# Kernel tuning notes

Measured on AMD Instinct MI355X. Metric: run time of the kernel, lower is better.

## Reference

```python
import jax, jax.numpy as jnp
import numpy as np

B, L, E, H, D, DFF = 2, 2048, 1024, 16, 64, 4096
SCALE = D ** 0.5


def rmsnorm(x):
    # NOTE: original uses mean(x*x)**0.5 with no eps and no learned scale
    rms = jnp.sqrt(jnp.mean(x * x, axis=-1, keepdims=True))
    return x / rms


def alibi_matrix():
    i = jnp.arange(L)
    dists = -jnp.abs(i[None, :] - i[:, None]).astype(jnp.float32)  # [L, L]
    slopes = 2.0 ** (-jnp.linspace(1.0, 8.0, H))                   # [H]
    alibi = slopes[:, None, None] * dists                          # [H, L, L]
    causal = jnp.tril(jnp.ones((L, L), dtype=bool))
    return jnp.where(causal[None], alibi, -jnp.inf)[None]          # [1, H, L, L]


def setup_inputs() -> dict:
    key = jax.random.key(0)
    ks = jax.random.split(key, 16)
    s = 0.02
    return {
        "X": jax.random.normal(ks[0], (B, L, E), jnp.float32),
        "encoder_out": jax.random.normal(ks[1], (B, L, E), jnp.float32),
        # self-attention params
        "Wqkv": jax.random.normal(ks[2], (E, 3 * H * D), jnp.float32) * s,
        "bqkv": jnp.zeros((3 * H * D,), jnp.float32),
        "Wo_sa": jax.random.normal(ks[3], (H * D, E), jnp.float32) * s,
        "bo_sa": jnp.zeros((E,), jnp.float32),
        # cross-attention params (computed by torch module but its forward returns X, so unused)
        "Wq": jax.random.normal(ks[4], (E, H * D), jnp.float32) * s,
        "bq": jnp.zeros((H * D,), jnp.float32),
        "Wkv": jax.random.normal(ks[5], (E, 2 * H * D), jnp.float32) * s,
        "bkv": jnp.zeros((2 * H * D,), jnp.float32),
        "Wo_ca": jax.random.normal(ks[6], (H * D, E), jnp.float32) * s,
        "bo_ca": jnp.zeros((E,), jnp.float32),
        # GLU FFN params (bias=False)
        "Ww": jax.random.normal(ks[7], (E, DFF), jnp.float32) * s,
        "Wv": jax.random.normal(ks[8], (E, DFF), jnp.float32) * s,
        "Wout": jax.random.normal(ks[9], (DFF, E), jnp.float32) * s,
    }


def reference(X, encoder_out, Wqkv, bqkv, Wo_sa, bo_sa, Wq, bq, Wkv, bkv,
              Wo_ca, bo_ca, Ww, Wv, Wout):
    alibi = alibi_matrix()

    # ---- self-attention (pre-norm + residual) ----
    h = rmsnorm(X)
    qkv = (h @ Wqkv + bqkv).reshape(B, L, H, 3, D)
    Q, K, V = qkv[..., 0, :], qkv[..., 1, :], qkv[..., 2, :]      # [B, L, H, D]
    scores = jnp.einsum('blhd,bmhd->bhlm', Q, K) / SCALE + alibi  # [B, H, L, L]
    attn = jax.nn.softmax(scores, axis=-1)
    ctx = jnp.einsum('bhlm,bmhd->blhd', attn, V).reshape(B, L, H * D)
    X = X + ctx @ Wo_sa + bo_sa

    # ---- cross-attention stage ----
    # Faithful to source: CrossAttention.forward returns its input X (the
    # normalized tensor) rather than the attention output, so this block is
    # X + rmsnorm(X). Cross-attn params never affect the output.
    X = X + rmsnorm(X)

    # ---- GLU FFN (pre-norm + residual), exact (erf) GELU as in torch F.gelu ----
    h = rmsnorm(X)
    ff = jax.nn.gelu(h @ Ww, approximate=False) * (h @ Wv)
    X = X + ff @ Wout
    return X
```

## Files before the change

kernel.cpp:

```cpp
#include <hip/hip_runtime.h>

#define B_SZ 2
#define L_SEQ 2048
#define E_DIM 1024
#define NH 16
#define DH 64
#define DFF_DIM 4096
#define ROWS (B_SZ * L_SEQ)
#define NCID 80

typedef __attribute__((ext_vector_type(8))) short short8;
typedef __attribute__((ext_vector_type(4))) float f32x4;

__device__ __forceinline__ short f2bf(float f) {
  unsigned u = __builtin_bit_cast(unsigned, f);
  u = (u + 0x7FFFu + ((u >> 16) & 1u)) >> 16;
  return (short)u;
}
__device__ __forceinline__ float bf2f(short s) {
  unsigned u = ((unsigned)(unsigned short)s) << 16;
  return __builtin_bit_cast(float, u);
}

__device__ __forceinline__ float fast_gelu(float x) {
  float ax = fabsf(x) * 0.70710678118654752f;
  float t = __builtin_amdgcn_rcpf(__builtin_fmaf(0.3275911f, ax, 1.0f));
  float p = t * __builtin_fmaf(
                    t,
                    __builtin_fmaf(
                        t,
                        __builtin_fmaf(t,
                                       __builtin_fmaf(t, 1.061405429f,
                                                      -1.453152027f),
                                       1.421413741f),
                        -0.284496736f),
                    0.254829592f);
  float erf = 1.0f - p * __expf(-ax * ax);
  erf = copysignf(erf, x);
  return 0.5f * x * (1.0f + erf);
}

__device__ __forceinline__ void async_copy16(const void* g, void* l) {
  __builtin_amdgcn_global_load_lds(
      (const __attribute__((address_space(1))) void*)g,
      (__attribute__((address_space(3))) void*)l, 16, 0, 0);
}

__device__ __forceinline__ float block_sum256(float v) {
  __shared__ float sbuf[4];
#pragma unroll
  for (int off = 32; off > 0; off >>= 1) v += __shfl_xor(v, off, 64);
  int lane = threadIdx.x & 63, w = threadIdx.x >> 6;
  if (lane == 0) sbuf[w] = v;
  __syncthreads();
  return sbuf[0] + sbuf[1] + sbuf[2] + sbuf[3];
}

__global__ __launch_bounds__(256) void prep_all(
    const float* __restrict__ Wqkv, const float* __restrict__ Wo,
    const float* __restrict__ Ww, const float* __restrict__ Wv,
    const float* __restrict__ Wout, const float* __restrict__ X,
    short* __restrict__ Bqkv3, short* __restrict__ WoT,
    short* __restrict__ Bcat, short* __restrict__ WoutT,
    short* __restrict__ H) {
  __shared__ float tile[32][33];
  int b = blockIdx.x;
  if (b < 16384) {
    const float* W;
    short* Wt;
    int K, N, mode, bx, by;
    if (b < 3072) {
      W = Wqkv; Wt = Bqkv3; K = 1024; N = 3072; mode = 1;
      bx = b % 96; by = b / 96;
    } else if (b < 4096) {
      int c = b - 3072;
      W = Wo; Wt = WoT; K = 1024; N = 1024; mode = 1;
      bx = c & 31; by = c >> 5;
    } else if (b < 8192) {
      int c = b - 4096;
      W = Ww; Wt = Bcat; K = 1024; N = 4096; mode = 2;
      bx = c & 127; by = c >> 7;
    } else if (b < 12288) {
      int c = b - 8192;
      W = Wv; Wt = Bcat; K = 1024; N = 4096; mode = 3;
      bx = c & 127; by = c >> 7;
    } else {
      int c = b - 12288;
      W = Wout; Wt = WoutT; K = 4096; N = 1024; mode = 1;
      bx = c & 31; by = c >> 5;
    }
    int n0 = bx * 32, k0 = by * 32;
    int tx = threadIdx.x & 31, ty = threadIdx.x >> 5;
#pragma unroll
    for (int i = 0; i < 4; i++)
      tile[ty + 8 * i][tx] = W[(size_t)(k0 + ty + 8 * i) * N + n0 + tx];
    __syncthreads();
#pragma unroll
    for (int i = 0; i < 4; i++) {
      int n = n0 + ty + 8 * i;
      int orow = (mode == 1)
                     ? n
                     : ((n >> 5) * 64 + (n & 31) + (mode == 3 ? 32 : 0));
      Wt[(size_t)orow * K + k0 + tx] = f2bf(tile[tx][ty + 8 * i]);
    }
  } else {
    size_t row = b - 16384;
    float4 v = ((const float4*)(X + row * E_DIM))[threadIdx.x];
    float ss = v.x * v.x + v.y * v.y + v.z * v.z + v.w * v.w;
    ss = block_sum256(ss);
    float inv = rsqrtf(ss * (1.0f / E_DIM));
    short* h = H + row * E_DIM + (size_t)threadIdx.x * 4;
    h[0] = f2bf(v.x * inv);
    h[1] = f2bf(v.y * inv);
    h[2] = f2bf(v.z * inv);
    h[3] = f2bf(v.w * inv);
  }
}

__global__ __launch_bounds__(256) void resid_rms_fused(
    const float* __restrict__ X, const float* __restrict__ P0,
    const float* __restrict__ P1, const float* __restrict__ bias,
    float* __restrict__ Xout, short* __restrict__ H) {
  size_t row = blockIdx.x;
  int t = threadIdx.x;
  float4 v = ((const float4*)(X + row * E_DIM))[t];
  float4 a = ((const float4*)(P0 + row * E_DIM))[t];
  float4 b = ((const float4*)(P1 + row * E_DIM))[t];
  float4 c = ((const float4*)bias)[t];
  v.x += a.x + b.x + c.x;
  v.y += a.y + b.y + c.y;
  v.z += a.z + b.z + c.z;
  v.w += a.w + b.w + c.w;
  float ss = v.x * v.x + v.y * v.y + v.z * v.z + v.w * v.w;
  ss = block_sum256(ss);
  float inv = rsqrtf(ss * (1.0f / E_DIM));
  float4 o;
  o.x = v.x * (1.0f + inv);
  o.y = v.y * (1.0f + inv);
  o.z = v.z * (1.0f + inv);
  o.w = v.w * (1.0f + inv);
  ((float4*)(Xout + row * E_DIM))[t] = o;
  short* h = H + row * E_DIM + (size_t)t * 4;
  h[0] = f2bf(v.x * inv);
  h[1] = f2bf(v.y * inv);
  h[2] = f2bf(v.z * inv);
  h[3] = f2bf(v.w * inv);
}

__global__ __launch_bounds__(256) void add2_k(const float* __restrict__ P0,
                                              const float* __restrict__ P1,
                                              float* __restrict__ out) {
  size_t i = (size_t)blockIdx.x * 256 + threadIdx.x;
  float4 v = ((const float4*)out)[i];
  float4 a = ((const float4*)P0)[i];
  float4 b = ((const float4*)P1)[i];
  v.x += a.x + b.x;
  v.y += a.y + b.y;
  v.z += a.z + b.z;
  v.w += a.w + b.w;
  ((float4*)out)[i] = v;
}

__global__ __launch_bounds__(256, 2) void gemm_bt(
    const short* __restrict__ A, const short* __restrict__ Bt,
    const float* __restrict__ bias, void* __restrict__ out,
    void* __restrict__ out2, void* __restrict__ out3, int M, int N, int K,
    int epi, int ksplit) {
  __shared__ short smem[128 * 32 * 4];
  short* As0 = smem;
  short* Bs0 = smem + 4096;
  short* As1 = smem + 8192;
  short* Bs1 = smem + 12288;
  int t = threadIdx.x;
  int lane = t & 63;
  int quad = lane >> 4, l16 = lane & 15;
  int wave = t >> 6;
  int wr = wave >> 1, wc = wave & 1;
  int m0 = blockIdx.y * 128, n0 = blockIdx.x * 128;
  int klen = K / ksplit;
  int kstart = blockIdx.z * klen;

  f32x4 acc[4][4];
#pragma unroll
  for (int i = 0; i < 4; i++)
#pragma unroll
    for (int j = 0; j < 4; j++) acc[i][j] = (f32x4){0.f, 0.f, 0.f, 0.f};

  for (int k0 = kstart; k0 < kstart + klen; k0 += 64) {
    __syncthreads();
#pragma unroll
    for (int p = 0; p < 2; p++) {
      int s = p * 256 + t;
      int mm = s >> 2, kk = (s & 3) * 8;
      const short* ag = A + (size_t)(m0 + mm) * K + k0 + kk;
      const short* bg = Bt + (size_t)(n0 + mm) * K + k0 + kk;
      async_copy16(ag, As0 + (size_t)s * 8);
      async_copy16(bg, Bs0 + (size_t)s * 8);
      async_copy16(ag + 32, As1 + (size_t)s * 8);
      async_copy16(bg + 32, Bs1 + (size_t)s * 8);
    }
    __syncthreads();
#pragma unroll
    for (int half = 0; half < 2; half++) {
      const short* As = half ? As1 : As0;
      const short* Bs = half ? Bs1 : Bs0;
      short8 af[4], bfv[4];
#pragma unroll
      for (int i = 0; i < 4; i++) {
        af[i] = *(const short8*)&As[(wr * 64 + i * 16 + l16) * 32 + quad * 8];
        bfv[i] = *(const short8*)&Bs[(wc * 64 + i * 16 + l16) * 32 + quad * 8];
      }
#pragma unroll
      for (int mi = 0; mi < 4; mi++)
#pragma unroll
        for (int ni = 0; ni < 4; ni++)
          acc[mi][ni] = __builtin_amdgcn_mfma_f32_16x16x32_bf16(
              af[mi], bfv[ni], acc[mi][ni], 0, 0, 0);
    }
  }

  if (epi == 5) {
    short* FF = (short*)out;
    int ffbase = blockIdx.x * 64 + wc * 32;
#pragma unroll
    for (int mi = 0; mi < 4; mi++)
#pragma unroll
      for (int ni = 0; ni < 2; ni++)
#pragma unroll
        for (int r = 0; r < 4; r++) {
          int rowl = wr * 64 + mi * 16 + quad * 4 + r;
          float g = fast_gelu(acc[mi][ni][r]);
          FF[(size_t)(m0 + rowl) * DFF_DIM + ffbase + ni * 16 + l16] =
              f2bf(g * acc[mi][ni + 2][r]);
        }
    return;
  }

#pragma unroll
  for (int mi = 0; mi < 4; mi++) {
#pragma unroll
    for (int ni = 0; ni < 4; ni++) {
      int col = n0 + wc * 64 + ni * 16 + l16;
#pragma unroll
      for (int r = 0; r < 4; r++) {
        int row = m0 + wr * 64 + mi * 16 + quad * 4 + r;
        float v = acc[mi][ni][r];
        if (epi == 4) {
          float* po = (float*)out + (size_t)blockIdx.z * ((size_t)M * N);
          po[(size_t)row * N + col] = v;
        } else {
          v += bias[col];
          int h = col / 192;
          int rem = col - h * 192;
          int ty = rem >> 6, d = rem & 63;
          short* dst = (ty == 0) ? (short*)out
                                 : ((ty == 1) ? (short*)out2 : (short*)out3);
          int bb = row >> 11, l = row & 2047;
          dst[((size_t)(bb * NH + h) * L_SEQ + l) * DH + d] = f2bf(v);
        }
      }
    }
  }
}

__global__ __launch_bounds__(256) void v_transp(const short* __restrict__ Vh,
                                                short* __restrict__ VTh) {
  int lt = blockIdx.x, bh = blockIdx.y;
  __shared__ short vtile[64 * 72];
  int t = threadIdx.x;
  int r = t >> 3, c = (t & 7) * 8;
  const short* src = Vh + ((size_t)bh * L_SEQ + lt * 64) * DH;
#pragma unroll
  for (int p = 0; p < 2; p++) {
    int row = r + p * 32;
    short8 vv = *(const short8*)(src + (size_t)row * DH + c);
    *(short8*)&vtile[row * 72 + c] = vv;
  }
  __syncthreads();
#pragma unroll
  for (int p = 0; p < 2; p++) {
    int d = r + p * 32;
    short8 o;
#pragma unroll
    for (int u = 0; u < 8; u++) o[u] = vtile[(c + u) * 72 + d];
    *(short8*)(VTh + ((size_t)bh * DH + d) * L_SEQ + lt * 64 + c) = o;
  }
}

__global__ __launch_bounds__(256) void attn_k(const short* __restrict__ Qh,
                                              const short* __restrict__ Kh,
                                              const short* __restrict__ VTh,
                                              float* __restrict__ OP,
                                              float* __restrict__ RS) {
  int cid = blockIdx.x;
  int bh = blockIdx.y;
  int b = bh >> 4, h = bh & 15;
  int qt, ch;
  if (cid < 8) {
    qt = cid; ch = 0;
  } else if (cid < 24) {
    qt = 8 + ((cid - 8) >> 1); ch = (cid - 8) & 1;
  } else if (cid < 48) {
    qt = 16 + (cid - 24) / 3; ch = (cid - 24) % 3;
  } else {
    qt = 24 + ((cid - 48) >> 2); ch = (cid - 48) & 3;
  }
  int t0 = ch * 8;
  int tend = min(t0 + 8, qt + 1);

  int t = threadIdx.x;
  int wave = t >> 6, lane = t & 63;
  int quad = lane >> 4, l16 = lane & 15;

  __shared__ short kt[64 * 72];
  __shared__ short vt[64 * 72];
  __shared__ short pb[4 * 16 * 70];

  const float slope = exp2f(-(1.0f + (7.0f / 15.0f) * (float)h));
  int iw = qt * 64 + wave * 16;

  short8 qf[2];
  {
    const short* qp = Qh + ((size_t)bh * L_SEQ + iw + l16) * DH + quad * 8;
    qf[0] = *(const short8*)(qp);
    qf[1] = *(const short8*)(qp + 32);
  }

  f32x4 o[4];
#pragma unroll
  for (int i = 0; i < 4; i++) o[i] = (f32x4){0.f, 0.f, 0.f, 0.f};
  float rs[4] = {0.f, 0.f, 0.f, 0.f};
  float crow[4];
  int irow[4];
#pragma unroll
  for (int r = 0; r < 4; r++) {
    irow[r] = iw + quad * 4 + r;
    crow[r] = -slope * (float)irow[r] - 8.0f;
  }

  int sr = t >> 3, sc = (t & 7) * 8;
  const short* kg = Kh + (size_t)bh * L_SEQ * DH;
  const short* vg = VTh + (size_t)bh * DH * L_SEQ;
  short8 kreg[2], vreg[2];
  auto loadKV = [&](int j0) {
    kreg[0] = *(const short8*)(kg + (size_t)(j0 + sr) * DH + sc);
    kreg[1] = *(const short8*)(kg + (size_t)(j0 + sr + 32) * DH + sc);
    vreg[0] = *(const short8*)(vg + (size_t)sr * L_SEQ + j0 + sc);
    vreg[1] = *(const short8*)(vg + (size_t)(sr + 32) * L_SEQ + j0 + sc);
  };
  loadKV(t0 * 64);

  short* pw = &pb[wave * 16 * 70];
  for (int tix = t0; tix < tend; ++tix) {
    int j0 = tix * 64;
    __syncthreads();
    *(short8*)&kt[sr * 72 + sc] = kreg[0];
    *(short8*)&kt[(sr + 32) * 72 + sc] = kreg[1];
    *(short8*)&vt[sr * 72 + sc] = vreg[0];
    *(short8*)&vt[(sr + 32) * 72 + sc] = vreg[1];
    __syncthreads();
    if (tix + 1 < tend) loadKV(j0 + 64);

    f32x4 s[4];
#pragma unroll
    for (int nt = 0; nt < 4; nt++) {
      f32x4 a = (f32x4){0.f, 0.f, 0.f, 0.f};
#pragma unroll
      for (int ks = 0; ks < 2; ks++) {
        short8 bf =
            *(const short8*)&kt[(nt * 16 + l16) * 72 + ks * 32 + quad * 8];
        a = __builtin_amdgcn_mfma_f32_16x16x32_bf16(qf[ks], bf, a, 0, 0, 0);
      }
      s[nt] = a;
    }
    bool diag = (tix == qt);
#pragma unroll
    for (int nt = 0; nt < 4; nt++) {
      int j = j0 + nt * 16 + l16;
      float jb = slope * (float)j;
#pragma unroll
      for (int r = 0; r < 4; r++) {
        float v = __builtin_fmaf(s[nt][r], 0.125f, jb + crow[r]);
        if (diag && j > irow[r]) v = -1e30f;
        float p = __expf(v);
        rs[r] += p;
        pw[(quad * 4 + r) * 70 + nt * 16 + l16] = f2bf(p);
      }
    }
    short8 pf[2];
    pf[0] = *(const short8*)&pw[l16 * 70 + quad * 8];
    pf[1] = *(const short8*)&pw[l16 * 70 + 32 + quad * 8];
#pragma unroll
    for (int nt = 0; nt < 4; nt++) {
#pragma unroll
      for (int ks = 0; ks < 2; ks++) {
        short8 bv =
            *(const short8*)&vt[(nt * 16 + l16) * 72 + ks * 32 + quad * 8];
        o[nt] = __builtin_amdgcn_mfma_f32_16x16x32_bf16(pf[ks], bv, o[nt], 0,
                                                        0, 0);
      }
    }
  }
  float* op = OP + ((size_t)bh * NCID + cid) * 64 * 64;
  float* rsp = RS + ((size_t)bh * NCID + cid) * 64;
#pragma unroll
  for (int r = 0; r < 4; r++) {
#pragma unroll
    for (int off = 1; off < 16; off <<= 1) rs[r] += __shfl_xor(rs[r], off, 64);
    int rowl = wave * 16 + quad * 4 + r;
#pragma unroll
    for (int nt = 0; nt < 4; nt++) op[rowl * 64 + nt * 16 + l16] = o[nt][r];
    if (l16 == 0) rsp[rowl] = rs[r];
  }
}

__global__ __launch_bounds__(256) void attn_merge(const float* __restrict__ OP,
                                                  const float* __restrict__ RS,
                                                  short* __restrict__ ctx) {
  int row = blockIdx.x;
  int b = row >> 11, i = row & 2047;
  int qt = i >> 6, rowin = i & 63;
  int base, nch;
  if (qt < 8) {
    base = qt; nch = 1;
  } else if (qt < 16) {
    base = 8 + 2 * (qt - 8); nch = 2;
  } else if (qt < 24) {
    base = 24 + 3 * (qt - 16); nch = 3;
  } else {
    base = 48 + 4 * (qt - 24); nch = 4;
  }
  int t = threadIdx.x;
  int col = t * 4;
  int h = col >> 6;
  int bh = b * NH + h;
  float4 o = {0.f, 0.f, 0.f, 0.f};
  float l = 0.f;
  for (int s = 0; s < nch; s++) {
    size_t cb = ((size_t)bh * NCID + base + s) * 64 + rowin;
    float4 v = *(const float4*)&OP[cb * 64 + (col & 63)];
    o.x += v.x;
    o.y += v.y;
    o.z += v.z;
    o.w += v.w;
    l += RS[cb];
  }
  float inv = 1.0f / l;
  short* dst = ctx + (size_t)row * (NH * DH) + col;
  dst[0] = f2bf(o.x * inv);
  dst[1] = f2bf(o.y * inv);
  dst[2] = f2bf(o.z * inv);
  dst[3] = f2bf(o.w * inv);
}

extern "C" void kernel_launch(void* const* d_in, const int* in_sizes, int n_in,
                              void* d_out, int out_size, void* d_ws,
                              size_t ws_size, hipStream_t stream) {
  const float* X = (const float*)d_in[0];
  const float* Wqkv = (const float*)d_in[2];
  const float* bqkv = (const float*)d_in[3];
  const float* Wo_sa = (const float*)d_in[4];
  const float* bo_sa = (const float*)d_in[5];
  const float* Ww = (const float*)d_in[12];
  const float* Wv = (const float*)d_in[13];
  const float* Wout = (const float*)d_in[14];

  char* ws = (char*)d_ws;
  auto take = [&](size_t bytes) {
    char* p = ws;
    ws += (bytes + 255) & ~(size_t)255;
    return p;
  };
  short* Bqkv3 = (short*)take((size_t)3072 * 1024 * 2);
  short* WoT = (short*)take((size_t)E_DIM * E_DIM * 2);
  short* Bcat = (short*)take((size_t)2 * DFF_DIM * E_DIM * 2);
  short* WoutT = (short*)take((size_t)E_DIM * DFF_DIM * 2);
  short* Hbuf = (short*)take((size_t)ROWS * E_DIM * 2);
  short* Qh = (short*)take((size_t)ROWS * NH * DH * 2);
  short* Kh = (short*)take((size_t)ROWS * NH * DH * 2);
  short* Vh = (short*)take((size_t)ROWS * NH * DH * 2);
  short* VTh = (short*)take((size_t)ROWS * NH * DH * 2);
  short* CTX = (short*)take((size_t)ROWS * NH * DH * 2);
  char* big = take((size_t)48 * 1024 * 1024);
  float* OP = (float*)big;
  float* RS = OP + (size_t)B_SZ * NH * NCID * 64 * 64;
  float* Pwo = (float*)(big + (size_t)16 * 1024 * 1024);
  short* FF = (short*)Pwo;
  float* Pwout = (float*)Qh;
  (void)ws_size;
  (void)in_sizes;
  (void)n_in;
  (void)out_size;

  dim3 blk(256);
  prep_all<<<16384 + ROWS, blk, 0, stream>>>(Wqkv, Wo_sa, Ww, Wv, Wout, X,
                                             Bqkv3, WoT, Bcat, WoutT, Hbuf);
  gemm_bt<<<dim3(3072 / 128, ROWS / 128), blk, 0, stream>>>(
      Hbuf, Bqkv3, bqkv, Qh, Kh, Vh, ROWS, 3072, 1024, 6, 1);
  v_transp<<<dim3(L_SEQ / 64, B_SZ * NH), blk, 0, stream>>>(Vh, VTh);
  attn_k<<<dim3(NCID, B_SZ * NH), blk, 0, stream>>>(Qh, Kh, VTh, OP, RS);
  attn_merge<<<ROWS, blk, 0, stream>>>(OP, RS, CTX);
  gemm_bt<<<dim3(1024 / 128, ROWS / 128, 2), blk, 0, stream>>>(
      CTX, WoT, nullptr, Pwo, nullptr, nullptr, ROWS, 1024, 1024, 4, 2);
  resid_rms_fused<<<ROWS, blk, 0, stream>>>(
      X, Pwo, Pwo + (size_t)ROWS * E_DIM, bo_sa, (float*)d_out, Hbuf);
  gemm_bt<<<dim3(2 * DFF_DIM / 128, ROWS / 128), blk, 0, stream>>>(
      Hbuf, Bcat, nullptr, FF, nullptr, nullptr, ROWS, 2 * DFF_DIM, 1024, 5,
      1);
  gemm_bt<<<dim3(1024 / 128, ROWS / 128, 2), blk, 0, stream>>>(
      FF, WoutT, nullptr, Pwout, nullptr, nullptr, ROWS, 1024, 4096, 4, 2);
  add2_k<<<ROWS * E_DIM / (256 * 4), blk, 0, stream>>>(
      Pwout, Pwout + (size_t)ROWS * E_DIM, (float*)d_out);
}
```

Measured before the change: 422.7 us.

## Switch GEMM to 32x32x16 MFMA with XOR-swizzled LDS tiles

```diff
diff --git a/kernel.cpp b/kernel.cpp
--- a/kernel.cpp
+++ b/kernel.cpp
@@ -11,6 +11,7 @@
 
 typedef __attribute__((ext_vector_type(8))) short short8;
 typedef __attribute__((ext_vector_type(4))) float f32x4;
+typedef __attribute__((ext_vector_type(16))) float f32x16;
 
 __device__ __forceinline__ short f2bf(float f) {
   unsigned u = __builtin_bit_cast(unsigned, f);
@@ -161,7 +162,7 @@
   ((float4*)out)[i] = v;
 }
 
-__global__ __launch_bounds__(256, 2) void gemm_bt(
+__global__ __launch_bounds__(256, 3) void gemm_bt(
     const short* __restrict__ A, const short* __restrict__ Bt,
     const float* __restrict__ bias, void* __restrict__ out,
     void* __restrict__ out2, void* __restrict__ out3, int M, int N, int K,
@@ -173,25 +174,34 @@
   short* Bs1 = smem + 12288;
   int t = threadIdx.x;
   int lane = t & 63;
-  int quad = lane >> 4, l16 = lane & 15;
+  int l31 = lane & 31, khalf = lane >> 5;
   int wave = t >> 6;
   int wr = wave >> 1, wc = wave & 1;
   int m0 = blockIdx.y * 128, n0 = blockIdx.x * 128;
   int klen = K / ksplit;
   int kstart = blockIdx.z * klen;
 
-  f32x4 acc[4][4];
-#pragma unroll
-  for (int i = 0; i < 4; i++)
-#pragma unroll
-    for (int j = 0; j < 4; j++) acc[i][j] = (f32x4){0.f, 0.f, 0.f, 0.f};
+  f32x16 acc[2][2];
+#pragma unroll
+  for (int i = 0; i < 2; i++)
+#pragma unroll
+    for (int j = 0; j < 2; j++)
+#pragma unroll
+      for (int e = 0; e < 16; e++) acc[i][j][e] = 0.f;
+
+  int rbaseA = (wr * 64 + l31) * 32;
+  int rbaseB = (wc * 64 + l31) * 32;
+  int ph[2];
+  ph[0] = ((khalf ^ (l31 & 3)) * 8);
+  ph[1] = (((2 + khalf) ^ (l31 & 3)) * 8);
 
   for (int k0 = kstart; k0 < kstart + klen; k0 += 64) {
     __syncthreads();
 #pragma unroll
     for (int p = 0; p < 2; p++) {
       int s = p * 256 + t;
-      int mm = s >> 2, kk = (s & 3) * 8;
+      int mm = s >> 2;
+      int kk = ((s & 3) ^ (mm & 3)) * 8;
       const short* ag = A + (size_t)(m0 + mm) * K + k0 + kk;
       const short* bg = Bt + (size_t)(n0 + mm) * K + k0 + kk;
       async_copy16(ag, As0 + (size_t)s * 8);
@@ -204,59 +214,65 @@
     for (int half = 0; half < 2; half++) {
       const short* As = half ? As1 : As0;
       const short* Bs = half ? Bs1 : Bs0;
-      short8 af[4], bfv[4];
-#pragma unroll
-      for (int i = 0; i < 4; i++) {
-        af[i] = *(const short8*)&As[(wr * 64 + i * 16 + l16) * 32 + quad * 8];
-        bfv[i] = *(const short8*)&Bs[(wc * 64 + i * 16 + l16) * 32 + quad * 8];
+#pragma unroll
+      for (int ks = 0; ks < 2; ks++) {
+        short8 a0 = *(const short8*)&As[rbaseA + ph[ks]];
+        short8 a1 = *(const short8*)&As[rbaseA + 1024 + ph[ks]];
+        short8 b0 = *(const short8*)&Bs[rbaseB + ph[ks]];
+        short8 b1 = *(const short8*)&Bs[rbaseB + 1024 + ph[ks]];
+        acc[0][0] = __builtin_amdgcn_mfma_f32_32x32x16_bf16(a0, b0, acc[0][0],
+                                                            0, 0, 0);
+        acc[0][1] = __builtin_amdgcn_mfma_f32_32x32x16_bf16(a0, b1, acc[0][1],
+                                                            0, 0, 0);
+        acc[1][0] = __builtin_amdgcn_mfma_f32_32x32x16_bf16(a1, b0, acc[1][0],
+                                                            0, 0, 0);
+        acc[1][1] = __builtin_amdgcn_mfma_f32_32x32x16_bf16(a1, b1, acc[1][1],
+                                                            0, 0, 0);
       }
-#pragma unroll
-      for (int mi = 0; mi < 4; mi++)
-#pragma unroll
-        for (int ni = 0; ni < 4; ni++)
-          acc[mi][ni] = __builtin_amdgcn_mfma_f32_16x16x32_bf16(
-              af[mi], bfv[ni], acc[mi][ni], 0, 0, 0);
     }
   }
 
   if (epi == 5) {
     short* FF = (short*)out;
-    int ffbase = blockIdx.x * 64 + wc * 32;
-#pragma unroll
-    for (int mi = 0; mi < 4; mi++)
-#pragma unroll
-      for (int ni = 0; ni < 2; ni++)
-#pragma unroll
-        for (int r = 0; r < 4; r++) {
-          int rowl = wr * 64 + mi * 16 + quad * 4 + r;
-          float g = fast_gelu(acc[mi][ni][r]);
-          FF[(size_t)(m0 + rowl) * DFF_DIM + ffbase + ni * 16 + l16] =
-              f2bf(g * acc[mi][ni + 2][r]);
+    int ffcol = blockIdx.x * 64 + wc * 32 + l31;
+#pragma unroll
+    for (int mi = 0; mi < 2; mi++)
+#pragma unroll
+      for (int r = 0; r < 16; r++) {
+        int row = m0 + wr * 64 + mi * 32 + (r & 3) + 8 * (r >> 2) + 4 * khalf;
+        float g = fast_gelu(acc[mi][0][r]);
+        FF[(size_t)row * DFF_DIM + ffcol] = f2bf(g * acc[mi][1][r]);
+      }
+    return;
+  }
+
+#pragma unroll
+  for (int mi = 0; mi < 2; mi++) {
+#pragma unroll
+    for (int ni = 0; ni < 2; ni++) {
+      int col = n0 + wc * 64 + ni * 32 + l31;
+      if (epi == 4) {
+        float* po = (float*)out + (size_t)blockIdx.z * ((size_t)M * N);
+#pragma unroll
+        for (int r = 0; r < 16; r++) {
+          int row =
+              m0 + wr * 64 + mi * 32 + (r & 3) + 8 * (r >> 2) + 4 * khalf;
+          po[(size_t)row * N + col] = acc[mi][ni][r];
         }
-    return;
-  }
-
-#pragma unroll
-  for (int mi = 0; mi < 4; mi++) {
-#pragma unroll
-    for (int ni = 0; ni < 4; ni++) {
-      int col = n0 + wc * 64 + ni * 16 + l16;
-#pragma unroll
-      for (int r = 0; r < 4; r++) {
-        int row = m0 + wr * 64 + mi * 16 + quad * 4 + r;
-        float v = acc[mi][ni][r];
-        if (epi == 4) {
-          float* po = (float*)out + (size_t)blockIdx.z * ((size_t)M * N);
-          po[(size_t)row * N + col] = v;
-        } else {
-          v += bias[col];
-          int h = col / 192;
-          int rem = col - h * 192;
-          int ty = rem >> 6, d = rem & 63;
-          short* dst = (ty == 0) ? (short*)out
-                                 : ((ty == 1) ? (short*)out2 : (short*)out3);
+      } else {
+        float bv = bias[col];
+        int h = col / 192;
+        int rem = col - h * 192;
+        int ty = rem >> 6, d = rem & 63;
+        short* dst = (ty == 0) ? (short*)out
+                               : ((ty == 1) ? (short*)out2 : (short*)out3);
+#pragma unroll
+        for (int r = 0; r < 16; r++) {
+          int row =
+              m0 + wr * 64 + mi * 32 + (r & 3) + 8 * (r >> 2) + 4 * khalf;
           int bb = row >> 11, l = row & 2047;
-          dst[((size_t)(bb * NH + h) * L_SEQ + l) * DH + d] = f2bf(v);
+          dst[((size_t)(bb * NH + h) * L_SEQ + l) * DH + d] =
+              f2bf(acc[mi][ni][r] + bv);
         }
       }
     }
```

New measurement: 441.7 us. 4.5% more time.
